# Kernel tuning notes

Hardware: AMD Instinct MI355X
Metric: run time of the kernel (lower is better)

The kernel has to match this reference:

```python
import jax, jax.numpy as jnp
import numpy as np

IDIM = 128
C = 3
NB_SAMPLES = 128
R = 32768
SH_C0 = 0.28209479177387814
SH_C1 = 0.4886025119029199
SH_C2 = np.array([1.0925484305920792, -1.0925484305920792, 0.31539156525252005,
                  -1.0925484305920792, 0.5462742152960396], dtype=np.float32)


def eval_sh_bases(d):
    # d: (R,3) unit directions -> (R,9) degree-2 real SH basis
    x, y, z = d[:, 0], d[:, 1], d[:, 2]
    return jnp.stack([
        jnp.full_like(x, SH_C0),
        -SH_C1 * y, SH_C1 * z, -SH_C1 * x,
        SH_C2[0] * x * y, SH_C2[1] * y * z,
        SH_C2[2] * (2.0 * z * z - x * x - y * y),
        SH_C2[3] * x * z, SH_C2[4] * (x * x - y * y)], axis=-1)


def trilerp(pts, grid):
    # pts: (N,3) in voxel coords (box_min=0, delta_voxel=1); grid: (D,D,D,F)
    D = grid.shape[0]
    p = jnp.clip(pts, 0.0, D - 1 - 1e-4)
    i0 = jnp.floor(p).astype(jnp.int32)
    w = p - i0.astype(p.dtype)          # (N,3) fractional weights
    i1 = jnp.minimum(i0 + 1, D - 1)
    out = jnp.zeros((pts.shape[0], grid.shape[-1]), dtype=p.dtype)
    for dx in (0, 1):
        wx = w[:, 0] if dx else 1.0 - w[:, 0]
        ix = i1[:, 0] if dx else i0[:, 0]
        for dy in (0, 1):
            wy = w[:, 1] if dy else 1.0 - w[:, 1]
            iy = i1[:, 1] if dy else i0[:, 1]
            for dz in (0, 1):
                wz = w[:, 2] if dz else 1.0 - w[:, 2]
                iz = i1[:, 2] if dz else i0[:, 2]
                out = out + (wx * wy * wz)[:, None] * grid[ix, iy, iz]
    return out


def setup_inputs() -> dict:
    key = jax.random.key(0)
    k = jax.random.split(key, 6)
    x = jax.random.uniform(k[0], (R, 3), jnp.float32) * (IDIM - 1)
    d = jax.random.normal(k[1], (R, 3), jnp.float32)
    d = d / jnp.linalg.norm(d, axis=1, keepdims=True)
    tmin = jax.random.uniform(k[2], (R,), jnp.float32) * 5.0
    tmax = tmin + 20.0 + jax.random.uniform(k[3], (R,), jnp.float32) * 80.0
    grid = jax.random.uniform(k[4], (IDIM, IDIM, IDIM, 9 * C), jnp.float32)
    opacity = jax.random.uniform(k[5], (IDIM, IDIM, IDIM, 1), jnp.float32)
    return {"x": x, "d": d, "tmin": tmin, "tmax": tmax, "grid": grid, "opacity": opacity}


def reference(x, d, tmin, tmax, grid, opacity):
    nb_rays = x.shape[0]
    # samples = arange(0.05, 0.95, 1/nb_samples): S entries
    S = int(np.floor(0.9 * NB_SAMPLES - 1e-6)) + 1
    base = 0.05 + jnp.arange(S, dtype=x.dtype) / NB_SAMPLES            # (S,)
    samples = (tmax - tmin)[:, None] * base[None, :] + tmin[:, None]   # (R,S)
    pts = x[:, None, :] + samples[..., None] * d[:, None, :]           # (R,S,3)
    sh = eval_sh_bases(d)                                              # (R,9)
    flat = pts.reshape(-1, 3)
    coeffs = trilerp(flat, grid).reshape(nb_rays, S, C, 9)             # (R,S,C,9)
    op = jnp.clip(trilerp(flat, opacity), 0.0, 100000.0).reshape(nb_rays, S)
    harm = coeffs * sh[:, None, None, :]                               # (R,S,C,9)
    samples_color = jnp.clip(harm.sum(axis=3) + 0.5, 0.0, 100000.0)    # (R,S,C)
    deltas = samples[:, 1:] - samples[:, :-1]                          # (R,S-1)
    dts = -(deltas * op[:, :-1])
    cum = jnp.concatenate([jnp.zeros((nb_rays, 1), dtype=x.dtype),
                           jnp.cumsum(dts, axis=1)[:, :-1]], axis=1)
    w = jnp.exp(cum) * (1.0 - jnp.exp(dts))                            # (R,S-1)
    rays_color = jnp.sum(w[..., None] * samples_color[:, :-1, :], axis=1)  # (R,C)
    return rays_color
```

## Files before the change

kernel.cpp:

```cpp
#include <hip/hip_runtime.h>

#define NS 115
#define WEPS 5e-5f
#define LOG_TSKIP -6.9078f
#define NCELLS (128*128*128)
#define PACK_BYTES ((size_t)NCELLS * 64)
#define NRAYS_C 32768
#define WBUF_BYTES ((size_t)NRAYS_C * 128 * 4)
#define NEED_BYTES (PACK_BYTES + WBUF_BYTES)
#define PACK_BLOCKS 2048
#define PACK_THREADS (PACK_BLOCKS * 256)
#define PACK_ITERS ((NCELLS * 4) / PACK_THREADS)

typedef float f32x4 __attribute__((ext_vector_type(4)));
typedef float f32x2 __attribute__((ext_vector_type(2)));
typedef _Float16 h16x8 __attribute__((ext_vector_type(8)));
typedef _Float16 h16x4 __attribute__((ext_vector_type(4)));

struct SH9 { float a,b,c,d,e,f,g,h,i; };

__device__ __forceinline__ f32x4 load4(const float* p) { f32x4 v; __builtin_memcpy(&v, p, 16); return v; }
__device__ __forceinline__ f32x2 load2(const float* p) { f32x2 v; __builtin_memcpy(&v, p, 8);  return v; }
__device__ __forceinline__ h16x8 load8h(const _Float16* p) { h16x8 v; __builtin_memcpy(&v, p, 16); return v; }
__device__ __forceinline__ h16x4 load4h(const _Float16* p) { h16x4 v; __builtin_memcpy(&v, p, 8);  return v; }
__device__ __forceinline__ f32x4 ntload4(const float* p) {
    return __builtin_nontemporal_load((const f32x4*)p);
}

__device__ __forceinline__ void pos_to_cell(float px, float py, float pz,
                                            int& ibase, float* wxs, float* wys, float* wzs) {
    px = fminf(fmaxf(px, 0.0f), 126.9999f);
    py = fminf(fmaxf(py, 0.0f), 126.9999f);
    pz = fminf(fmaxf(pz, 0.0f), 126.9999f);
    int ix = (int)px, iy = (int)py, iz = (int)pz;
    float wx = px - (float)ix, wy = py - (float)iy, wz = pz - (float)iz;
    ibase = (ix << 14) + (iy << 7) + iz;
    wxs[0] = 1.0f - wx; wxs[1] = wx;
    wys[0] = 1.0f - wy; wys[1] = wy;
    wzs[0] = 1.0f - wz; wzs[1] = wz;
}

__device__ __forceinline__ float eval_op(float px, float py, float pz,
                                         const float* __restrict__ opa) {
    int ibase; float wxs[2], wys[2], wzs[2];
    pos_to_cell(px, py, pz, ibase, wxs, wys, wzs);
    float op = 0.0f;
    #pragma unroll
    for (int cx = 0; cx < 2; ++cx)
    #pragma unroll
    for (int cy = 0; cy < 2; ++cy) {
        int idx = ibase + (cx << 14) + (cy << 7);
        f32x2 pr = load2(opa + idx);
        float wxy = wxs[cx] * wys[cy];
        op = fmaf(wxy * wzs[0], pr.x, op);
        op = fmaf(wxy * wzs[1], pr.y, op);
    }
    return fminf(fmaxf(op, 0.0f), 100000.0f);
}

__device__ __forceinline__ void eval_color_h(float px, float py, float pz,
                                             const _Float16* __restrict__ pack,
                                             const SH9& sh,
                                             float& cr, float& cg, float& cb) {
    int ibase; float wxs[2], wys[2], wzs[2];
    pos_to_cell(px, py, pz, ibase, wxs, wys, wzs);
    float r = 0.0f, g = 0.0f, b = 0.0f;
    #pragma unroll
    for (int cx = 0; cx < 2; ++cx)
    #pragma unroll
    for (int cy = 0; cy < 2; ++cy)
    #pragma unroll
    for (int cz = 0; cz < 2; ++cz) {
        int idx = ibase + (cx << 14) + (cy << 7) + cz;
        float wc = wxs[cx] * wys[cy] * wzs[cz];
        const _Float16* cp = pack + ((size_t)idx << 5);
        h16x8 v0 = load8h(cp);
        h16x8 v1 = load8h(cp + 8);
        h16x8 v2 = load8h(cp + 16);
        h16x4 v3 = load4h(cp + 24);
        float c0 = sh.a*(float)v0[0] + sh.b*(float)v0[1] + sh.c*(float)v0[2] + sh.d*(float)v0[3]
                 + sh.e*(float)v0[4] + sh.f*(float)v0[5] + sh.g*(float)v0[6] + sh.h*(float)v0[7]
                 + sh.i*(float)v1[0];
        float c1 = sh.a*(float)v1[1] + sh.b*(float)v1[2] + sh.c*(float)v1[3] + sh.d*(float)v1[4]
                 + sh.e*(float)v1[5] + sh.f*(float)v1[6] + sh.g*(float)v1[7] + sh.h*(float)v2[0]
                 + sh.i*(float)v2[1];
        float c2 = sh.a*(float)v2[2] + sh.b*(float)v2[3] + sh.c*(float)v2[4] + sh.d*(float)v2[5]
                 + sh.e*(float)v2[6] + sh.f*(float)v2[7] + sh.g*(float)v3[0] + sh.h*(float)v3[1]
                 + sh.i*(float)v3[2];
        r = fmaf(wc, c0, r);
        g = fmaf(wc, c1, g);
        b = fmaf(wc, c2, b);
    }
    cr = fminf(fmaxf(r + 0.5f, 0.0f), 100000.0f);
    cg = fminf(fmaxf(g + 0.5f, 0.0f), 100000.0f);
    cb = fminf(fmaxf(b + 0.5f, 0.0f), 100000.0f);
}

__device__ __forceinline__ void eval_color_f(float px, float py, float pz,
                                             const float* __restrict__ grid,
                                             const SH9& sh,
                                             float& cr, float& cg, float& cb) {
    int ibase; float wxs[2], wys[2], wzs[2];
    pos_to_cell(px, py, pz, ibase, wxs, wys, wzs);
    float r = 0.0f, g = 0.0f, b = 0.0f;
    #pragma unroll
    for (int cx = 0; cx < 2; ++cx)
    #pragma unroll
    for (int cy = 0; cy < 2; ++cy)
    #pragma unroll
    for (int cz = 0; cz < 2; ++cz) {
        int idx = ibase + (cx << 14) + (cy << 7) + cz;
        float wc = wxs[cx] * wys[cy] * wzs[cz];
        const float* cp = grid + (size_t)idx * 27;
        f32x4 v0 = load4(cp);
        f32x4 v1 = load4(cp + 4);
        f32x4 v2 = load4(cp + 8);
        f32x4 v3 = load4(cp + 12);
        f32x4 v4 = load4(cp + 16);
        f32x4 v5 = load4(cp + 20);
        f32x4 v6 = load4(cp + 23);
        float c0 = sh.a*v0.x + sh.b*v0.y + sh.c*v0.z + sh.d*v0.w
                 + sh.e*v1.x + sh.f*v1.y + sh.g*v1.z + sh.h*v1.w + sh.i*v2.x;
        float c1 = sh.a*v2.y + sh.b*v2.z + sh.c*v2.w + sh.d*v3.x
                 + sh.e*v3.y + sh.f*v3.z + sh.g*v3.w + sh.h*v4.x + sh.i*v4.y;
        float c2 = sh.a*v4.z + sh.b*v4.w + sh.c*v5.x + sh.d*v5.y
                 + sh.e*v5.z + sh.f*v5.w + sh.g*v6.y + sh.h*v6.z + sh.i*v6.w;
        r = fmaf(wc, c0, r);
        g = fmaf(wc, c1, g);
        b = fmaf(wc, c2, b);
    }
    cr = fminf(fmaxf(r + 0.5f, 0.0f), 100000.0f);
    cg = fminf(fmaxf(g + 0.5f, 0.0f), 100000.0f);
    cb = fminf(fmaxf(b + 0.5f, 0.0f), 100000.0f);
}

__device__ __forceinline__ float wave_incl_scan(float v, int lane) {
    #pragma unroll
    for (int off = 1; off < 64; off <<= 1) {
        float n = __shfl_up(v, (unsigned)off, 64);
        if (lane >= off) v += n;
    }
    return v;
}

__device__ __forceinline__ SH9 make_sh(float ddx, float ddy, float ddz) {
    SH9 sh;
    sh.a = 0.28209479177387814f;
    sh.b = -0.4886025119029199f * ddy;
    sh.c =  0.4886025119029199f * ddz;
    sh.d = -0.4886025119029199f * ddx;
    sh.e =  1.0925484305920792f * ddx * ddy;
    sh.f = -1.0925484305920792f * ddy * ddz;
    sh.g =  0.31539156525252005f * (2.0f*ddz*ddz - ddx*ddx - ddy*ddy);
    sh.h = -1.0925484305920792f * ddx * ddz;
    sh.i =  0.5462742152960396f * (ddx*ddx - ddy*ddy);
    return sh;
}

__device__ __forceinline__ void pack_one(const float* __restrict__ grid,
                                         _Float16* __restrict__ pack, int o) {
    int cell = o >> 2;
    int q = o & 3;
    int base = cell * 27;
    int offa = base + ((q == 3) ? 23 : q * 8);
    int offb = (q == 3) ? offa : offa + 4;
    f32x4 a = ntload4(grid + offa);
    f32x4 b = ntload4(grid + offb);
    h16x8 out;
    if (q == 3) {
        out[0] = (_Float16)a.y; out[1] = (_Float16)a.z; out[2] = (_Float16)a.w;
        out[3] = (_Float16)0.f; out[4] = (_Float16)0.f; out[5] = (_Float16)0.f;
        out[6] = (_Float16)0.f; out[7] = (_Float16)0.f;
    } else {
        out[0] = (_Float16)a.x; out[1] = (_Float16)a.y; out[2] = (_Float16)a.z; out[3] = (_Float16)a.w;
        out[4] = (_Float16)b.x; out[5] = (_Float16)b.y; out[6] = (_Float16)b.z; out[7] = (_Float16)b.w;
    }
    __builtin_memcpy(pack + ((size_t)o << 3), &out, 16);
}

__global__ __launch_bounds__(256) void pack_op_kernel(
    const float* __restrict__ grid, _Float16* __restrict__ pack,
    const float* __restrict__ x, const float* __restrict__ d,
    const float* __restrict__ tmin, const float* __restrict__ tmax,
    const float* __restrict__ opa, float* __restrict__ wbuf, int nrays)
{
    const int t = threadIdx.x;
    const int tid = blockIdx.x * 256 + t;

    #pragma unroll 1
    for (int i = 0; i < PACK_ITERS; i += 8) {
        #pragma unroll
        for (int j = 0; j < 8; ++j)
            pack_one(grid, pack, tid + (i + j) * PACK_THREADS);
    }

    const int wave = tid >> 6;
    const int lane = t & 63;
    #pragma unroll 1
    for (int r = 0; r < 4; ++r) {
        int ray = __builtin_amdgcn_readfirstlane(wave * 4 + r);
        if (ray >= nrays) break;
        float ox = x[3*ray+0], oy = x[3*ray+1], oz = x[3*ray+2];
        float ddx = d[3*ray+0], ddy = d[3*ray+1], ddz = d[3*ray+2];
        float t0 = tmin[ray], t1 = tmax[ray];
        float range = t1 - t0;
        float delta = range * 0.0078125f;

        float tt = range * (0.05f + (float)lane * 0.0078125f) + t0;
        float px = ox + tt*ddx, py = oy + tt*ddy, pz = oz + tt*ddz;
        float opv = eval_op(px, py, pz, opa);
        float dts = -delta * opv;
        float incl = wave_incl_scan(dts, lane);
        float cum = incl - dts;
        float total0 = __shfl(incl, 63, 64);
        float w = __expf(cum) * (1.0f - __expf(dts));
        wbuf[ray * 128 + lane] = w;

        float w1 = 0.0f;
        if (total0 > LOG_TSKIP) {
            int s1 = 64 + lane;
            float dts1 = 0.0f;
            if (s1 < NS) {
                float t1s = range * (0.05f + (float)s1 * 0.0078125f) + t0;
                float qx = ox + t1s*ddx, qy = oy + t1s*ddy, qz = oz + t1s*ddz;
                dts1 = -delta * eval_op(qx, qy, qz, opa);
            }
            float incl1 = wave_incl_scan(dts1, lane);
            float cum1 = total0 + incl1 - dts1;
            w1 = __expf(cum1) * (1.0f - __expf(dts1));
        }
        wbuf[ray * 128 + 64 + lane] = w1;
    }
}

__global__ __launch_bounds__(256) void color_kernel(
    const float* __restrict__ x, const float* __restrict__ d,
    const float* __restrict__ tmin, const float* __restrict__ tmax,
    const _Float16* __restrict__ pack, const float* __restrict__ wbuf,
    float* __restrict__ out, int nrays)
{
    int gtid = blockIdx.x * blockDim.x + threadIdx.x;
    int ray = __builtin_amdgcn_readfirstlane(gtid >> 6);
    int lane = threadIdx.x & 63;
    if (ray >= nrays) return;

    float ox = x[3*ray+0], oy = x[3*ray+1], oz = x[3*ray+2];
    float ddx = d[3*ray+0], ddy = d[3*ray+1], ddz = d[3*ray+2];
    float t0 = tmin[ray], t1 = tmax[ray];
    float range = t1 - t0;
    SH9 sh = make_sh(ddx, ddy, ddz);

    float w0 = wbuf[ray * 128 + lane];
    float w1 = wbuf[ray * 128 + 64 + lane];

    float accR = 0.0f, accG = 0.0f, accB = 0.0f;
    if (w0 > WEPS) {
        float tt = range * (0.05f + (float)lane * 0.0078125f) + t0;
        float px = ox + tt*ddx, py = oy + tt*ddy, pz = oz + tt*ddz;
        float cr, cg, cb;
        eval_color_h(px, py, pz, pack, sh, cr, cg, cb);
        accR = w0 * cr; accG = w0 * cg; accB = w0 * cb;
    }
    if (w1 > WEPS) {
        float t1s = range * (0.05f + (float)(64 + lane) * 0.0078125f) + t0;
        float px = ox + t1s*ddx, py = oy + t1s*ddy, pz = oz + t1s*ddz;
        float cr, cg, cb;
        eval_color_h(px, py, pz, pack, sh, cr, cg, cb);
        accR = fmaf(w1, cr, accR);
        accG = fmaf(w1, cg, accG);
        accB = fmaf(w1, cb, accB);
    }

    #pragma unroll
    for (int off = 32; off > 0; off >>= 1) {
        accR += __shfl_xor(accR, off, 64);
        accG += __shfl_xor(accG, off, 64);
        accB += __shfl_xor(accB, off, 64);
    }
    if (lane == 0) {
        out[3*ray+0] = accR;
        out[3*ray+1] = accG;
        out[3*ray+2] = accB;
    }
}

__global__ __launch_bounds__(256) void rf_fallback(
    const float* __restrict__ x, const float* __restrict__ d,
    const float* __restrict__ tmin, const float* __restrict__ tmax,
    const float* __restrict__ grid, const float* __restrict__ opa,
    float* __restrict__ out, int nrays)
{
    int gtid = blockIdx.x * blockDim.x + threadIdx.x;
    int ray = __builtin_amdgcn_readfirstlane(gtid >> 6);
    int lane = threadIdx.x & 63;
    if (ray >= nrays) return;

    float ox = x[3*ray+0], oy = x[3*ray+1], oz = x[3*ray+2];
    float ddx = d[3*ray+0], ddy = d[3*ray+1], ddz = d[3*ray+2];
    float t0 = tmin[ray], t1 = tmax[ray];
    float range = t1 - t0;
    float delta = range * 0.0078125f;
    SH9 sh = make_sh(ddx, ddy, ddz);

    float accR = 0.0f, accG = 0.0f, accB = 0.0f;
    {
        float tt = range * (0.05f + (float)lane * 0.0078125f) + t0;
        float px = ox + tt*ddx, py = oy + tt*ddy, pz = oz + tt*ddz;
        float opv = eval_op(px, py, pz, opa);
        float dts = -delta * opv;
        float incl = wave_incl_scan(dts, lane);
        float cum = incl - dts;
        float total0 = __shfl(incl, 63, 64);
        float w = __expf(cum) * (1.0f - __expf(dts));
        if (w > WEPS) {
            float cr, cg, cb;
            eval_color_f(px, py, pz, grid, sh, cr, cg, cb);
            accR = w * cr; accG = w * cg; accB = w * cb;
        }
        if (total0 > LOG_TSKIP) {
            int s1 = 64 + lane;
            float dts1 = 0.0f;
            float px1 = 0.f, py1 = 0.f, pz1 = 0.f;
            if (s1 < NS) {
                float t1s = range * (0.05f + (float)s1 * 0.0078125f) + t0;
                px1 = ox + t1s*ddx; py1 = oy + t1s*ddy; pz1 = oz + t1s*ddz;
                dts1 = -delta * eval_op(px1, py1, pz1, opa);
            }
            float incl1 = wave_incl_scan(dts1, lane);
            float cum1 = total0 + incl1 - dts1;
            float w1 = __expf(cum1) * (1.0f - __expf(dts1));
            if (w1 > WEPS) {
                float cr, cg, cb;
                eval_color_f(px1, py1, pz1, grid, sh, cr, cg, cb);
                accR = fmaf(w1, cr, accR);
                accG = fmaf(w1, cg, accG);
                accB = fmaf(w1, cb, accB);
            }
        }
    }
    #pragma unroll
    for (int off = 32; off > 0; off >>= 1) {
        accR += __shfl_xor(accR, off, 64);
        accG += __shfl_xor(accG, off, 64);
        accB += __shfl_xor(accB, off, 64);
    }
    if (lane == 0) {
        out[3*ray+0] = accR;
        out[3*ray+1] = accG;
        out[3*ray+2] = accB;
    }
}

extern "C" void kernel_launch(void* const* d_in, const int* in_sizes, int n_in,
                              void* d_out, int out_size, void* d_ws, size_t ws_size,
                              hipStream_t stream) {
    const float* x    = (const float*)d_in[0];
    const float* d    = (const float*)d_in[1];
    const float* tmin = (const float*)d_in[2];
    const float* tmax = (const float*)d_in[3];
    const float* grid = (const float*)d_in[4];
    const float* opa  = (const float*)d_in[5];
    float* out = (float*)d_out;

    int nrays = in_sizes[0] / 3;
    int blocks = (nrays * 64 + 255) / 256;

    if (ws_size >= NEED_BYTES && nrays <= NRAYS_C) {
        _Float16* pack = (_Float16*)d_ws;
        float* wbuf = (float*)((char*)d_ws + PACK_BYTES);
        pack_op_kernel<<<PACK_BLOCKS, 256, 0, stream>>>(grid, pack, x, d, tmin, tmax, opa, wbuf, nrays);
        color_kernel<<<blocks, 256, 0, stream>>>(x, d, tmin, tmax, pack, wbuf, out, nrays);
    } else {
        rf_fallback<<<blocks, 256, 0, stream>>>(x, d, tmin, tmax, grid, opa, out, nrays);
    }
}
```

Baseline: 403.7 us.

## Split pack and opacity work into separate block roles, interleave two rays

Even-numbered blocks of the first kernel now only repack the grid to fp16, and odd-numbered blocks only compute opacity transmittance weights, so the two jobs overlap across blocks instead of running back to back in every thread. Each opacity wave handles eight rays, two at a time, so the trilinear gathers and scans of both rays can be in flight together. Pack blocks now do twice as many iterations each. The gain depends on how the scheduler mixes the two block types, and processing two rays at once raises register pressure.

```diff
diff --git a/kernel.cpp b/kernel.cpp
--- a/kernel.cpp
+++ b/kernel.cpp
@@ -8,9 +8,12 @@
 #define NRAYS_C 32768
 #define WBUF_BYTES ((size_t)NRAYS_C * 128 * 4)
 #define NEED_BYTES (PACK_BYTES + WBUF_BYTES)
-#define PACK_BLOCKS 2048
+#define TOTAL_BLOCKS 2048
+#define PACK_BLOCKS 1024
 #define PACK_THREADS (PACK_BLOCKS * 256)
 #define PACK_ITERS ((NCELLS * 4) / PACK_THREADS)
+#define OP_WAVES (PACK_BLOCKS * 4)
+#define RAYS_PER_OPWAVE 8
 
 typedef float f32x4 __attribute__((ext_vector_type(4)));
 typedef float f32x2 __attribute__((ext_vector_type(2)));
@@ -178,6 +181,21 @@
     __builtin_memcpy(pack + ((size_t)o << 3), &out, 16);
 }
 
+struct RayP { float ox,oy,oz,dx,dy,dz,t0,range,delta; };
+
+__device__ __forceinline__ RayP load_ray(const float* __restrict__ x,
+                                         const float* __restrict__ d,
+                                         const float* __restrict__ tmin,
+                                         const float* __restrict__ tmax, int ray) {
+    RayP r;
+    r.ox = x[3*ray+0]; r.oy = x[3*ray+1]; r.oz = x[3*ray+2];
+    r.dx = d[3*ray+0]; r.dy = d[3*ray+1]; r.dz = d[3*ray+2];
+    r.t0 = tmin[ray];
+    r.range = tmax[ray] - r.t0;
+    r.delta = r.range * 0.0078125f;
+    return r;
+}
+
 __global__ __launch_bounds__(256) void pack_op_kernel(
     const float* __restrict__ grid, _Float16* __restrict__ pack,
     const float* __restrict__ x, const float* __restrict__ d,
@@ -185,51 +203,84 @@
     const float* __restrict__ opa, float* __restrict__ wbuf, int nrays)
 {
     const int t = threadIdx.x;
-    const int tid = blockIdx.x * 256 + t;
+    const int role_id = blockIdx.x >> 1;
+
+    if ((blockIdx.x & 1) == 0) {
+        const int tid = role_id * 256 + t;
+        #pragma unroll 1
+        for (int i = 0; i < PACK_ITERS; i += 8) {
+            #pragma unroll
+            for (int j = 0; j < 8; ++j)
+                pack_one(grid, pack, tid + (i + j) * PACK_THREADS);
+        }
+        return;
+    }
+
+    const int otid = role_id * 256 + t;
+    const int wave = otid >> 6;
+    const int lane = t & 63;
+    const int rbase = wave * RAYS_PER_OPWAVE;
+    const float fl = (float)lane;
 
     #pragma unroll 1
-    for (int i = 0; i < PACK_ITERS; i += 8) {
-        #pragma unroll
-        for (int j = 0; j < 8; ++j)
-            pack_one(grid, pack, tid + (i + j) * PACK_THREADS);
-    }
-
-    const int wave = tid >> 6;
-    const int lane = t & 63;
-    #pragma unroll 1
-    for (int r = 0; r < 4; ++r) {
-        int ray = __builtin_amdgcn_readfirstlane(wave * 4 + r);
-        if (ray >= nrays) break;
-        float ox = x[3*ray+0], oy = x[3*ray+1], oz = x[3*ray+2];
-        float ddx = d[3*ray+0], ddy = d[3*ray+1], ddz = d[3*ray+2];
-        float t0 = tmin[ray], t1 = tmax[ray];
-        float range = t1 - t0;
-        float delta = range * 0.0078125f;
-
-        float tt = range * (0.05f + (float)lane * 0.0078125f) + t0;
-        float px = ox + tt*ddx, py = oy + tt*ddy, pz = oz + tt*ddz;
-        float opv = eval_op(px, py, pz, opa);
-        float dts = -delta * opv;
-        float incl = wave_incl_scan(dts, lane);
-        float cum = incl - dts;
-        float total0 = __shfl(incl, 63, 64);
-        float w = __expf(cum) * (1.0f - __expf(dts));
-        wbuf[ray * 128 + lane] = w;
-
-        float w1 = 0.0f;
-        if (total0 > LOG_TSKIP) {
+    for (int p = 0; p < RAYS_PER_OPWAVE / 2; ++p) {
+        int rayA = __builtin_amdgcn_readfirstlane(rbase + 2 * p);
+        if (rayA >= nrays) break;
+        int rayBr = rayA + 1;
+        bool hasB = rayBr < nrays;
+        int rayB = hasB ? rayBr : rayA;
+
+        RayP A = load_ray(x, d, tmin, tmax, rayA);
+        RayP B = load_ray(x, d, tmin, tmax, rayB);
+
+        float ttA = A.range * (0.05f + fl * 0.0078125f) + A.t0;
+        float ttB = B.range * (0.05f + fl * 0.0078125f) + B.t0;
+        float pxA = A.ox + ttA*A.dx, pyA = A.oy + ttA*A.dy, pzA = A.oz + ttA*A.dz;
+        float pxB = B.ox + ttB*B.dx, pyB = B.oy + ttB*B.dy, pzB = B.oz + ttB*B.dz;
+        float opA = eval_op(pxA, pyA, pzA, opa);
+        float opB = eval_op(pxB, pyB, pzB, opa);
+        float dtsA = -A.delta * opA;
+        float dtsB = -B.delta * opB;
+        float inclA = wave_incl_scan(dtsA, lane);
+        float inclB = wave_incl_scan(dtsB, lane);
+        float cumA = inclA - dtsA;
+        float cumB = inclB - dtsB;
+        float totalA = __shfl(inclA, 63, 64);
+        float totalB = __shfl(inclB, 63, 64);
+        wbuf[rayA * 128 + lane] = __expf(cumA) * (1.0f - __expf(dtsA));
+        if (hasB) wbuf[rayB * 128 + lane] = __expf(cumB) * (1.0f - __expf(dtsB));
+
+        float w1A = 0.0f;
+        if (totalA > LOG_TSKIP) {
             int s1 = 64 + lane;
             float dts1 = 0.0f;
             if (s1 < NS) {
-                float t1s = range * (0.05f + (float)s1 * 0.0078125f) + t0;
-                float qx = ox + t1s*ddx, qy = oy + t1s*ddy, qz = oz + t1s*ddz;
-                dts1 = -delta * eval_op(qx, qy, qz, opa);
+                float t1s = A.range * (0.05f + (float)s1 * 0.0078125f) + A.t0;
+                float qx = A.ox + t1s*A.dx, qy = A.oy + t1s*A.dy, qz = A.oz + t1s*A.dz;
+                dts1 = -A.delta * eval_op(qx, qy, qz, opa);
             }
             float incl1 = wave_incl_scan(dts1, lane);
-            float cum1 = total0 + incl1 - dts1;
-            w1 = __expf(cum1) * (1.0f - __expf(dts1));
+            float cum1 = totalA + incl1 - dts1;
+            w1A = __expf(cum1) * (1.0f - __expf(dts1));
         }
-        wbuf[ray * 128 + 64 + lane] = w1;
+        wbuf[rayA * 128 + 64 + lane] = w1A;
+
+        if (hasB) {
+            float w1B = 0.0f;
+            if (totalB > LOG_TSKIP) {
+                int s1 = 64 + lane;
+                float dts1 = 0.0f;
+                if (s1 < NS) {
+                    float t1s = B.range * (0.05f + (float)s1 * 0.0078125f) + B.t0;
+                    float qx = B.ox + t1s*B.dx, qy = B.oy + t1s*B.dy, qz = B.oz + t1s*B.dz;
+                    dts1 = -B.delta * eval_op(qx, qy, qz, opa);
+                }
+                float incl1 = wave_incl_scan(dts1, lane);
+                float cum1 = totalB + incl1 - dts1;
+                w1B = __expf(cum1) * (1.0f - __expf(dts1));
+            }
+            wbuf[rayB * 128 + 64 + lane] = w1B;
+        }
     }
 }
 
@@ -368,7 +419,7 @@
     if (ws_size >= NEED_BYTES && nrays <= NRAYS_C) {
         _Float16* pack = (_Float16*)d_ws;
         float* wbuf = (float*)((char*)d_ws + PACK_BYTES);
-        pack_op_kernel<<<PACK_BLOCKS, 256, 0, stream>>>(grid, pack, x, d, tmin, tmax, opa, wbuf, nrays);
+        pack_op_kernel<<<TOTAL_BLOCKS, 256, 0, stream>>>(grid, pack, x, d, tmin, tmax, opa, wbuf, nrays);
         color_kernel<<<blocks, 256, 0, stream>>>(x, d, tmin, tmax, pack, wbuf, out, nrays);
     } else {
         rf_fallback<<<blocks, 256, 0, stream>>>(x, d, tmin, tmax, grid, opa, out, nrays);
```

Result: slower. 421.6 us (+4.4%).

## Split each sample's color gather across four lanes and skip empty 16-sample groups

Applied to the files above, without the earlier changes.

The color kernel now assigns four lanes per sample, each loading one 16-byte slice of the packed fp16 SH coefficients per corner and computing a partial dot product with a lane-specific SH weight selection; partials are combined with xor shuffles. Samples are processed in eight groups of 16, and groups where no sample has significant weight are skipped via ballot masks. This is meant to make loads more coalesced and compact the work onto active samples instead of diverging per lane. It adds shuffle overhead and zero-padded multiply work per lane, plus a serial loop of up to eight iterations.

```diff
diff --git a/kernel.cpp b/kernel.cpp
--- a/kernel.cpp
+++ b/kernel.cpp
@@ -56,44 +56,6 @@
         op = fmaf(wxy * wzs[1], pr.y, op);
     }
     return fminf(fmaxf(op, 0.0f), 100000.0f);
-}
-
-__device__ __forceinline__ void eval_color_h(float px, float py, float pz,
-                                             const _Float16* __restrict__ pack,
-                                             const SH9& sh,
-                                             float& cr, float& cg, float& cb) {
-    int ibase; float wxs[2], wys[2], wzs[2];
-    pos_to_cell(px, py, pz, ibase, wxs, wys, wzs);
-    float r = 0.0f, g = 0.0f, b = 0.0f;
-    #pragma unroll
-    for (int cx = 0; cx < 2; ++cx)
-    #pragma unroll
-    for (int cy = 0; cy < 2; ++cy)
-    #pragma unroll
-    for (int cz = 0; cz < 2; ++cz) {
-        int idx = ibase + (cx << 14) + (cy << 7) + cz;
-        float wc = wxs[cx] * wys[cy] * wzs[cz];
-        const _Float16* cp = pack + ((size_t)idx << 5);
-        h16x8 v0 = load8h(cp);
-        h16x8 v1 = load8h(cp + 8);
-        h16x8 v2 = load8h(cp + 16);
-        h16x4 v3 = load4h(cp + 24);
-        float c0 = sh.a*(float)v0[0] + sh.b*(float)v0[1] + sh.c*(float)v0[2] + sh.d*(float)v0[3]
-                 + sh.e*(float)v0[4] + sh.f*(float)v0[5] + sh.g*(float)v0[6] + sh.h*(float)v0[7]
-                 + sh.i*(float)v1[0];
-        float c1 = sh.a*(float)v1[1] + sh.b*(float)v1[2] + sh.c*(float)v1[3] + sh.d*(float)v1[4]
-                 + sh.e*(float)v1[5] + sh.f*(float)v1[6] + sh.g*(float)v1[7] + sh.h*(float)v2[0]
-                 + sh.i*(float)v2[1];
-        float c2 = sh.a*(float)v2[2] + sh.b*(float)v2[3] + sh.c*(float)v2[4] + sh.d*(float)v2[5]
-                 + sh.e*(float)v2[6] + sh.f*(float)v2[7] + sh.g*(float)v3[0] + sh.h*(float)v3[1]
-                 + sh.i*(float)v3[2];
-        r = fmaf(wc, c0, r);
-        g = fmaf(wc, c1, g);
-        b = fmaf(wc, c2, b);
-    }
-    cr = fminf(fmaxf(r + 0.5f, 0.0f), 100000.0f);
-    cg = fminf(fmaxf(g + 0.5f, 0.0f), 100000.0f);
-    cb = fminf(fmaxf(b + 0.5f, 0.0f), 100000.0f);
 }
 
 __device__ __forceinline__ void eval_color_f(float px, float py, float pz,
@@ -243,36 +205,87 @@
     int ray = __builtin_amdgcn_readfirstlane(gtid >> 6);
     int lane = threadIdx.x & 63;
     if (ray >= nrays) return;
+    int qd  = lane >> 2;
+    int sub = lane & 3;
 
     float ox = x[3*ray+0], oy = x[3*ray+1], oz = x[3*ray+2];
     float ddx = d[3*ray+0], ddy = d[3*ray+1], ddz = d[3*ray+2];
-    float t0 = tmin[ray], t1 = tmax[ray];
-    float range = t1 - t0;
+    float t0 = tmin[ray];
+    float range = tmax[ray] - t0;
     SH9 sh = make_sh(ddx, ddy, ddz);
+
+    float s00,s01,s02,s03,s04,s05,s06,s07;
+    float s10,s11,s12,s13,s14,s15,s16,s17;
+    if (sub == 0) {
+        s00=sh.a;s01=sh.b;s02=sh.c;s03=sh.d;s04=sh.e;s05=sh.f;s06=sh.g;s07=sh.h;
+        s10=0.f;s11=0.f;s12=0.f;s13=0.f;s14=0.f;s15=0.f;s16=0.f;s17=0.f;
+    } else if (sub == 1) {
+        s00=sh.i;s01=0.f;s02=0.f;s03=0.f;s04=0.f;s05=0.f;s06=0.f;s07=0.f;
+        s10=0.f;s11=sh.a;s12=sh.b;s13=sh.c;s14=sh.d;s15=sh.e;s16=sh.f;s17=sh.g;
+    } else if (sub == 2) {
+        s00=sh.h;s01=sh.i;s02=0.f;s03=0.f;s04=0.f;s05=0.f;s06=0.f;s07=0.f;
+        s10=0.f;s11=0.f;s12=sh.a;s13=sh.b;s14=sh.c;s15=sh.d;s16=sh.e;s17=sh.f;
+    } else {
+        s00=sh.g;s01=sh.h;s02=sh.i;s03=0.f;s04=0.f;s05=0.f;s06=0.f;s07=0.f;
+        s10=0.f;s11=0.f;s12=0.f;s13=0.f;s14=0.f;s15=0.f;s16=0.f;s17=0.f;
+    }
 
     float w0 = wbuf[ray * 128 + lane];
     float w1 = wbuf[ray * 128 + 64 + lane];
+    unsigned long long b0 = __ballot(w0 > WEPS);
+    unsigned long long b1 = __ballot(w1 > WEPS);
 
     float accR = 0.0f, accG = 0.0f, accB = 0.0f;
-    if (w0 > WEPS) {
-        float tt = range * (0.05f + (float)lane * 0.0078125f) + t0;
-        float px = ox + tt*ddx, py = oy + tt*ddy, pz = oz + tt*ddz;
-        float cr, cg, cb;
-        eval_color_h(px, py, pz, pack, sh, cr, cg, cb);
-        accR = w0 * cr; accG = w0 * cg; accB = w0 * cb;
-    }
-    if (w1 > WEPS) {
-        float t1s = range * (0.05f + (float)(64 + lane) * 0.0078125f) + t0;
-        float px = ox + t1s*ddx, py = oy + t1s*ddy, pz = oz + t1s*ddz;
-        float cr, cg, cb;
-        eval_color_h(px, py, pz, pack, sh, cr, cg, cb);
-        accR = fmaf(w1, cr, accR);
-        accG = fmaf(w1, cg, accG);
-        accB = fmaf(w1, cb, accB);
-    }
-
-    #pragma unroll
-    for (int off = 32; off > 0; off >>= 1) {
+
+    #pragma unroll 1
+    for (int p = 0; p < 8; ++p) {
+        unsigned long long bsel = (p < 4) ? b0 : b1;
+        int shl = (p & 3) << 4;
+        if (((bsel >> shl) & 0xFFFFull) == 0) continue;
+        int s = (p << 4) + qd;
+        float ws = __shfl((p < 4) ? w0 : w1, s & 63, 64);
+        if (ws > WEPS) {
+            float tt = range * (0.05f + (float)s * 0.0078125f) + t0;
+            float px = ox + tt*ddx, py = oy + tt*ddy, pz = oz + tt*ddz;
+            int ibase; float wxs[2], wys[2], wzs[2];
+            pos_to_cell(px, py, pz, ibase, wxs, wys, wzs);
+            float d0a = 0.0f, d1a = 0.0f;
+            #pragma unroll
+            for (int cx = 0; cx < 2; ++cx)
+            #pragma unroll
+            for (int cy = 0; cy < 2; ++cy)
+            #pragma unroll
+            for (int cz = 0; cz < 2; ++cz) {
+                int idx = ibase + (cx << 14) + (cy << 7) + cz;
+                float wc = wxs[cx] * wys[cy] * wzs[cz];
+                const _Float16* cp = pack + ((size_t)idx << 5) + (sub << 3);
+                h16x8 v = load8h(cp);
+                float f0=(float)v[0], f1=(float)v[1], f2=(float)v[2], f3=(float)v[3];
+                float f4=(float)v[4], f5=(float)v[5], f6=(float)v[6], f7=(float)v[7];
+                float e0 = s00*f0 + s01*f1 + s02*f2 + s03*f3
+                         + s04*f4 + s05*f5 + s06*f6 + s07*f7;
+                float e1 = s10*f0 + s11*f1 + s12*f2 + s13*f3
+                         + s14*f4 + s15*f5 + s16*f6 + s17*f7;
+                d0a = fmaf(wc, e0, d0a);
+                d1a = fmaf(wc, e1, d1a);
+            }
+            float rp = (sub < 2)  ? d0a : 0.0f;
+            float gp = (sub == 1) ? d1a : ((sub == 2) ? d0a : 0.0f);
+            float bp = (sub == 2) ? d1a : ((sub == 3) ? d0a : 0.0f);
+            rp += __shfl_xor(rp, 1, 64); rp += __shfl_xor(rp, 2, 64);
+            gp += __shfl_xor(gp, 1, 64); gp += __shfl_xor(gp, 2, 64);
+            bp += __shfl_xor(bp, 1, 64); bp += __shfl_xor(bp, 2, 64);
+            float cr = fminf(fmaxf(rp + 0.5f, 0.0f), 100000.0f);
+            float cg = fminf(fmaxf(gp + 0.5f, 0.0f), 100000.0f);
+            float cb = fminf(fmaxf(bp + 0.5f, 0.0f), 100000.0f);
+            accR = fmaf(ws, cr, accR);
+            accG = fmaf(ws, cg, accG);
+            accB = fmaf(ws, cb, accB);
+        }
+    }
+
+    #pragma unroll
+    for (int off = 4; off < 64; off <<= 1) {
         accR += __shfl_xor(accR, off, 64);
         accG += __shfl_xor(accG, off, 64);
         accB += __shfl_xor(accB, off, 64);
```

After: 401.6 us. No clear change (-0.5%).
